# Optimization experiments

Measured on AMD Instinct MI355X. Metric: run time of the kernel, lower is better.

The kernel has to match this reference:

```python
import jax, jax.numpy as jnp
import numpy as np


def setup_inputs() -> dict:
    key = jax.random.key(0)
    z = jax.random.normal(key, (8, 4096, 1024), dtype=jnp.float32)
    return {"z": z}


def reference(z):
    d = z.shape[-1]
    # sort descending along last dim
    z_sorted = -jnp.sort(-z, axis=-1)
    z_cumsum = jnp.cumsum(z_sorted, axis=-1)
    k = jnp.arange(1, d + 1, dtype=z.dtype)  # [d]
    rhs = 1 + k * z_sorted
    is_gt = (rhs > z_cumsum).astype(z.dtype)
    # largest k satisfying the support condition
    k_z = jnp.max(is_gt * k, axis=-1, keepdims=True)  # [..., 1]
    idx = k_z.astype(jnp.int32) - 1
    z_cumsum_k = jnp.take_along_axis(z_cumsum, idx, axis=-1)
    tau = (z_cumsum_k - 1) / k_z
    p = jnp.clip(z - tau, 0.0, None)
    return p
```

## Files before the change

kernel.cpp:

```cpp
#include <hip/hip_runtime.h>


#define ROW_D 1024

typedef float f4 __attribute__((ext_vector_type(4)));

template <int CTRL, int RMASK>
__device__ __forceinline__ float dpp_mv(float x) {
    return __builtin_bit_cast(float, __builtin_amdgcn_update_dpp(
        __builtin_bit_cast(int, x), __builtin_bit_cast(int, x),
        CTRL, RMASK, 0xf, false));
}

__device__ __forceinline__ float dpp_sum_to63(float x) {
    x += dpp_mv<0x111, 0xf>(x);
    x += dpp_mv<0x112, 0xf>(x);
    x += dpp_mv<0x114, 0xf>(x);
    x += dpp_mv<0x118, 0xf>(x);
    x += dpp_mv<0x142, 0xa>(x);
    x += dpp_mv<0x143, 0xc>(x);
    return x;
}
__device__ __forceinline__ float dpp_max_to63(float x) {
    x = fmaxf(x, dpp_mv<0x111, 0xf>(x));
    x = fmaxf(x, dpp_mv<0x112, 0xf>(x));
    x = fmaxf(x, dpp_mv<0x114, 0xf>(x));
    x = fmaxf(x, dpp_mv<0x118, 0xf>(x));
    x = fmaxf(x, dpp_mv<0x142, 0xa>(x));
    x = fmaxf(x, dpp_mv<0x143, 0xc>(x));
    return x;
}
__device__ __forceinline__ float bcast63(float x) {
    return __builtin_bit_cast(float,
        __builtin_amdgcn_readlane(__builtin_bit_cast(int, x), 63));
}
__device__ __forceinline__ float fast_rcp(float x) {
    float r;
    asm("v_rcp_f32 %0, %1" : "=v"(r) : "v"(x));
    return r;
}

__device__ __forceinline__ void ce(float& a, float& b) {
    const float hi = fmaxf(a, b);
    const float lo = fminf(a, b);
    a = hi; b = lo;
}
__device__ __forceinline__ void sort4(float& a, float& b, float& c, float& d) {
    ce(a, b); ce(c, d); ce(a, c); ce(b, d); ce(b, c);
}
__device__ __forceinline__ void merge44_top4(
    float A0, float A1, float A2, float A3,
    float B0, float B1, float B2, float B3,
    float& R0, float& R1, float& R2, float& R3) {
    float e0 = A0, e1 = A2, e2 = B0, e3 = B2;
    ce(e0, e2); ce(e1, e3); ce(e1, e2);
    float o0 = A1, o1 = A3, o2 = B1, o3 = B3;
    ce(o0, o2); ce(o1, o3); ce(o1, o2);
    R0 = e0;
    float x = o0, y = e1;
    ce(x, y);
    R1 = x; R2 = y;
    R3 = fmaxf(o1, e2);
}

__global__ __launch_bounds__(256) void sparsemax_kernel(
    const float* __restrict__ z, float* __restrict__ out, int nrows) {
    const int lane = (int)(threadIdx.x & 63u);
    const int row  = (int)(blockIdx.x << 2) + (int)(threadIdx.x >> 6);
    if (row >= nrows) return;

    const f4* __restrict__ zin = reinterpret_cast<const f4*>(z + (size_t)row * ROW_D);
    f4* __restrict__ pout      = reinterpret_cast<f4*>(out + (size_t)row * ROW_D);

    f4 v[4];
#pragma unroll
    for (int j = 0; j < 4; ++j) v[j] = zin[lane + 64 * j];

    float g[4][4];
#pragma unroll
    for (int j = 0; j < 4; ++j) {
        g[j][0] = v[j].x; g[j][1] = v[j].y; g[j][2] = v[j].z; g[j][3] = v[j].w;
        sort4(g[j][0], g[j][1], g[j][2], g[j][3]);
    }
    float a0, a1, a2, a3, b0, b1, b2, b3, T0, T1, T2, T3;
    merge44_top4(g[0][0], g[0][1], g[0][2], g[0][3],
                 g[1][0], g[1][1], g[1][2], g[1][3], a0, a1, a2, a3);
    merge44_top4(g[2][0], g[2][1], g[2][2], g[2][3],
                 g[3][0], g[3][1], g[3][2], g[3][3], b0, b1, b2, b3);
    merge44_top4(a0, a1, a2, a3, b0, b1, b2, b3, T0, T1, T2, T3);

    const float m = bcast63(dpp_max_to63(T0));
    float t = m - 1.0f;

    const unsigned long long bad = __ballot(T3 > t);
    if (bad == 0ull) {
#pragma unroll 1
        for (int it = 0; it < 16; ++it) {
            const float d0 = T0 - t, d1 = T1 - t, d2 = T2 - t, d3 = T3 - t;
            const float Sl = (fmaxf(d0, 0.0f) + fmaxf(d1, 0.0f)) +
                             (fmaxf(d2, 0.0f) + fmaxf(d3, 0.0f));
            int n = __popcll(__ballot(d0 > 0.0f));
            n += __popcll(__ballot(d1 > 0.0f));
            n += __popcll(__ballot(d2 > 0.0f));
            n += __popcll(__ballot(d3 > 0.0f));
            const float S = bcast63(dpp_sum_to63(Sl));
            const float step = (S - 1.0f) * fast_rcp((float)n);
            t += step;
            if (step <= 1e-6f) break;
        }
    } else {
#pragma unroll 1
        for (int it = 0; it < 16; ++it) {
            float sj[4];
            int n = 0;
#pragma unroll
            for (int j = 0; j < 4; ++j) {
                const float d0 = v[j].x - t, d1 = v[j].y - t;
                const float d2 = v[j].z - t, d3 = v[j].w - t;
                sj[j] = (fmaxf(d0, 0.0f) + fmaxf(d1, 0.0f)) +
                        (fmaxf(d2, 0.0f) + fmaxf(d3, 0.0f));
                n += __popcll(__ballot(d0 > 0.0f));
                n += __popcll(__ballot(d1 > 0.0f));
                n += __popcll(__ballot(d2 > 0.0f));
                n += __popcll(__ballot(d3 > 0.0f));
            }
            const float S = bcast63(dpp_sum_to63((sj[0] + sj[1]) + (sj[2] + sj[3])));
            const float step = (S - 1.0f) * fast_rcp((float)n);
            t += step;
            if (step <= 1e-6f) break;
        }
    }

#pragma unroll
    for (int j = 0; j < 4; ++j) {
        f4 o;
        o.x = fmaxf(v[j].x - t, 0.0f);
        o.y = fmaxf(v[j].y - t, 0.0f);
        o.z = fmaxf(v[j].z - t, 0.0f);
        o.w = fmaxf(v[j].w - t, 0.0f);
        pout[lane + 64 * j] = o;
    }
}

extern "C" void kernel_launch(void* const* d_in, const int* in_sizes, int n_in,
                              void* d_out, int out_size, void* d_ws, size_t ws_size,
                              hipStream_t stream) {
    const float* z = (const float*)d_in[0];
    float* out = (float*)d_out;
    const int n = in_sizes[0];
    const int nrows = n / ROW_D;
    const int blocks = (nrows + 3) / 4;
    sparsemax_kernel<<<blocks, 256, 0, stream>>>(z, out, nrows);
}
```

Before: 226.6 us.

## Map each row to a 16-lane group instead of a full wavefront

New measurement: 238.7 us. 5.3% more time.

```diff
diff --git a/kernel.cpp b/kernel.cpp
--- a/kernel.cpp
+++ b/kernel.cpp
@@ -12,27 +12,24 @@
         CTRL, RMASK, 0xf, false));
 }
 
-__device__ __forceinline__ float dpp_sum_to63(float x) {
+__device__ __forceinline__ float grp_bcast15(float x) {
+    return __builtin_bit_cast(float, __builtin_amdgcn_ds_swizzle(
+        __builtin_bit_cast(int, x), 0x1F0));
+}
+
+__device__ __forceinline__ float grp_sum16(float x) {
     x += dpp_mv<0x111, 0xf>(x);
     x += dpp_mv<0x112, 0xf>(x);
     x += dpp_mv<0x114, 0xf>(x);
     x += dpp_mv<0x118, 0xf>(x);
-    x += dpp_mv<0x142, 0xa>(x);
-    x += dpp_mv<0x143, 0xc>(x);
-    return x;
+    return grp_bcast15(x);
 }
-__device__ __forceinline__ float dpp_max_to63(float x) {
+__device__ __forceinline__ float grp_max16(float x) {
     x = fmaxf(x, dpp_mv<0x111, 0xf>(x));
     x = fmaxf(x, dpp_mv<0x112, 0xf>(x));
     x = fmaxf(x, dpp_mv<0x114, 0xf>(x));
     x = fmaxf(x, dpp_mv<0x118, 0xf>(x));
-    x = fmaxf(x, dpp_mv<0x142, 0xa>(x));
-    x = fmaxf(x, dpp_mv<0x143, 0xc>(x));
-    return x;
-}
-__device__ __forceinline__ float bcast63(float x) {
-    return __builtin_bit_cast(float,
-        __builtin_amdgcn_readlane(__builtin_bit_cast(int, x), 63));
+    return grp_bcast15(x);
 }
 __device__ __forceinline__ float fast_rcp(float x) {
     float r;
@@ -66,79 +63,74 @@
 __global__ __launch_bounds__(256) void sparsemax_kernel(
     const float* __restrict__ z, float* __restrict__ out, int nrows) {
     const int lane = (int)(threadIdx.x & 63u);
-    const int row  = (int)(blockIdx.x << 2) + (int)(threadIdx.x >> 6);
+    const int g    = lane >> 4;
+    const int p    = lane & 15;
+    const int wid  = (int)(blockIdx.x << 2) + (int)(threadIdx.x >> 6);
+    const int row  = (wid << 2) + g;
     if (row >= nrows) return;
 
-    const f4* __restrict__ zin = reinterpret_cast<const f4*>(z + (size_t)row * ROW_D);
-    f4* __restrict__ pout      = reinterpret_cast<f4*>(out + (size_t)row * ROW_D);
+    const f4* __restrict__ zrow = reinterpret_cast<const f4*>(z + (size_t)row * ROW_D);
+    f4* __restrict__ prow       = reinterpret_cast<f4*>(out + (size_t)row * ROW_D);
 
-    f4 v[4];
+    f4 v[16];
 #pragma unroll
-    for (int j = 0; j < 4; ++j) v[j] = zin[lane + 64 * j];
+    for (int j = 0; j < 16; ++j) v[j] = zrow[p + 16 * j];
 
-    float g[4][4];
+    float R0 = v[0].x, R1 = v[0].y, R2 = v[0].z, R3 = v[0].w;
+    sort4(R0, R1, R2, R3);
 #pragma unroll
-    for (int j = 0; j < 4; ++j) {
-        g[j][0] = v[j].x; g[j][1] = v[j].y; g[j][2] = v[j].z; g[j][3] = v[j].w;
-        sort4(g[j][0], g[j][1], g[j][2], g[j][3]);
+    for (int j = 1; j < 16; ++j) {
+        float c0 = v[j].x, c1 = v[j].y, c2 = v[j].z, c3 = v[j].w;
+        sort4(c0, c1, c2, c3);
+        merge44_top4(R0, R1, R2, R3, c0, c1, c2, c3, R0, R1, R2, R3);
     }
-    float a0, a1, a2, a3, b0, b1, b2, b3, T0, T1, T2, T3;
-    merge44_top4(g[0][0], g[0][1], g[0][2], g[0][3],
-                 g[1][0], g[1][1], g[1][2], g[1][3], a0, a1, a2, a3);
-    merge44_top4(g[2][0], g[2][1], g[2][2], g[2][3],
-                 g[3][0], g[3][1], g[3][2], g[3][3], b0, b1, b2, b3);
-    merge44_top4(a0, a1, a2, a3, b0, b1, b2, b3, T0, T1, T2, T3);
 
-    const float m = bcast63(dpp_max_to63(T0));
+    const float m = grp_max16(R0);
     float t = m - 1.0f;
 
-    const unsigned long long bad = __ballot(T3 > t);
-    if (bad == 0ull) {
+    if (__ballot(R3 > t) == 0ull) {
 #pragma unroll 1
         for (int it = 0; it < 16; ++it) {
-            const float d0 = T0 - t, d1 = T1 - t, d2 = T2 - t, d3 = T3 - t;
+            const float d0 = R0 - t, d1 = R1 - t, d2 = R2 - t, d3 = R3 - t;
             const float Sl = (fmaxf(d0, 0.0f) + fmaxf(d1, 0.0f)) +
                              (fmaxf(d2, 0.0f) + fmaxf(d3, 0.0f));
-            int n = __popcll(__ballot(d0 > 0.0f));
-            n += __popcll(__ballot(d1 > 0.0f));
-            n += __popcll(__ballot(d2 > 0.0f));
-            n += __popcll(__ballot(d3 > 0.0f));
-            const float S = bcast63(dpp_sum_to63(Sl));
-            const float step = (S - 1.0f) * fast_rcp((float)n);
+            const float Cl = ((d0 > 0.0f ? 1.0f : 0.0f) + (d1 > 0.0f ? 1.0f : 0.0f)) +
+                             ((d2 > 0.0f ? 1.0f : 0.0f) + (d3 > 0.0f ? 1.0f : 0.0f));
+            const float S = grp_sum16(Sl);
+            const float C = grp_sum16(Cl);
+            const float step = (S - 1.0f) * fast_rcp(C);
             t += step;
-            if (step <= 1e-6f) break;
+            if (__ballot(step > 1e-6f) == 0ull) break;
         }
     } else {
 #pragma unroll 1
         for (int it = 0; it < 16; ++it) {
-            float sj[4];
-            int n = 0;
+            float Sl = 0.0f, Cl = 0.0f;
 #pragma unroll
-            for (int j = 0; j < 4; ++j) {
+            for (int j = 0; j < 16; ++j) {
                 const float d0 = v[j].x - t, d1 = v[j].y - t;
                 const float d2 = v[j].z - t, d3 = v[j].w - t;
-                sj[j] = (fmaxf(d0, 0.0f) + fmaxf(d1, 0.0f)) +
-                        (fmaxf(d2, 0.0f) + fmaxf(d3, 0.0f));
-                n += __popcll(__ballot(d0 > 0.0f));
-                n += __popcll(__ballot(d1 > 0.0f));
-                n += __popcll(__ballot(d2 > 0.0f));
-                n += __popcll(__ballot(d3 > 0.0f));
+                Sl += (fmaxf(d0, 0.0f) + fmaxf(d1, 0.0f)) +
+                      (fmaxf(d2, 0.0f) + fmaxf(d3, 0.0f));
+                Cl += ((d0 > 0.0f ? 1.0f : 0.0f) + (d1 > 0.0f ? 1.0f : 0.0f)) +
+                      ((d2 > 0.0f ? 1.0f : 0.0f) + (d3 > 0.0f ? 1.0f : 0.0f));
             }
-            const float S = bcast63(dpp_sum_to63((sj[0] + sj[1]) + (sj[2] + sj[3])));
-            const float step = (S - 1.0f) * fast_rcp((float)n);
+            const float S = grp_sum16(Sl);
+            const float C = grp_sum16(Cl);
+            const float step = (S - 1.0f) * fast_rcp(C);
             t += step;
-            if (step <= 1e-6f) break;
+            if (__ballot(step > 1e-6f) == 0ull) break;
         }
     }
 
 #pragma unroll
-    for (int j = 0; j < 4; ++j) {
+    for (int j = 0; j < 16; ++j) {
         f4 o;
         o.x = fmaxf(v[j].x - t, 0.0f);
         o.y = fmaxf(v[j].y - t, 0.0f);
         o.z = fmaxf(v[j].z - t, 0.0f);
         o.w = fmaxf(v[j].w - t, 0.0f);
-        pout[lane + 64 * j] = o;
+        prow[p + 16 * j] = o;
     }
 }
 
@@ -149,6 +141,6 @@
     float* out = (float*)d_out;
     const int n = in_sizes[0];
     const int nrows = n / ROW_D;
-    const int blocks = (nrows + 3) / 4;
+    const int blocks = (nrows + 15) / 16;
     sparsemax_kernel<<<blocks, 256, 0, stream>>>(z, out, nrows);
 }
```

## Make kernel persistent with async global-to-LDS double-buffered row prefetch

Applied to the files above, without the earlier changes.

After: 229.9 us. No clear change (+1.5%).

```diff
diff --git a/kernel.cpp b/kernel.cpp
--- a/kernel.cpp
+++ b/kernel.cpp
@@ -63,19 +63,20 @@
     R3 = fmaxf(o1, e2);
 }
 
-__global__ __launch_bounds__(256) void sparsemax_kernel(
-    const float* __restrict__ z, float* __restrict__ out, int nrows) {
-    const int lane = (int)(threadIdx.x & 63u);
-    const int row  = (int)(blockIdx.x << 2) + (int)(threadIdx.x >> 6);
-    if (row >= nrows) return;
-
-    const f4* __restrict__ zin = reinterpret_cast<const f4*>(z + (size_t)row * ROW_D);
-    f4* __restrict__ pout      = reinterpret_cast<f4*>(out + (size_t)row * ROW_D);
-
-    f4 v[4];
-#pragma unroll
-    for (int j = 0; j < 4; ++j) v[j] = zin[lane + 64 * j];
-
+__device__ __forceinline__ void prefetch_row(const float* __restrict__ z,
+                                             int row, int lane,
+                                             float* ldsbase) {
+    const char* g = (const char*)(z + (size_t)row * ROW_D) + (size_t)lane * 16;
+#pragma unroll
+    for (int j = 0; j < 4; ++j) {
+        __builtin_amdgcn_global_load_lds(
+            (const __attribute__((address_space(1))) void*)(g + j * 1024),
+            (__attribute__((address_space(3))) void*)(ldsbase + j * 256),
+            16, 0, 0);
+    }
+}
+
+__device__ __forceinline__ float solve_tau(const f4 (&v)[4]) {
     float g[4][4];
 #pragma unroll
     for (int j = 0; j < 4; ++j) {
@@ -92,8 +93,7 @@
     const float m = bcast63(dpp_max_to63(T0));
     float t = m - 1.0f;
 
-    const unsigned long long bad = __ballot(T3 > t);
-    if (bad == 0ull) {
+    if (__ballot(T3 > t) == 0ull) {
 #pragma unroll 1
         for (int it = 0; it < 16; ++it) {
             const float d0 = T0 - t, d1 = T1 - t, d2 = T2 - t, d3 = T3 - t;
@@ -130,7 +130,13 @@
             if (step <= 1e-6f) break;
         }
     }
-
+    return t;
+}
+
+__device__ __forceinline__ void store_row(const f4 (&v)[4], float t,
+                                          float* __restrict__ out,
+                                          int row, int lane) {
+    f4* __restrict__ p = reinterpret_cast<f4*>(out + (size_t)row * ROW_D);
 #pragma unroll
     for (int j = 0; j < 4; ++j) {
         f4 o;
@@ -138,7 +144,47 @@
         o.y = fmaxf(v[j].y - t, 0.0f);
         o.z = fmaxf(v[j].z - t, 0.0f);
         o.w = fmaxf(v[j].w - t, 0.0f);
-        pout[lane + 64 * j] = o;
+        p[lane + 64 * j] = o;
+    }
+}
+
+__global__ __launch_bounds__(256) void sparsemax_kernel(
+    const float* __restrict__ z, float* __restrict__ out, int nrows) {
+    const int lane = (int)(threadIdx.x & 63u);
+    const int w    = (int)(threadIdx.x >> 6);
+    int r = (int)(blockIdx.x << 2) + w;
+    const int W = (int)(gridDim.x << 2);
+    if (r >= nrows) return;
+
+    __shared__ float lds[4][2][ROW_D];
+
+    f4 v[4];
+    {
+        const f4* __restrict__ zin = reinterpret_cast<const f4*>(z + (size_t)r * ROW_D);
+#pragma unroll
+        for (int j = 0; j < 4; ++j) v[j] = zin[lane + 64 * j];
+    }
+    int rn = r + W;
+    int s = 0;
+    if (rn < nrows) prefetch_row(z, rn, lane, &lds[w][0][0]);
+    __builtin_amdgcn_sched_barrier(0);
+
+    for (;;) {
+        const float t = solve_tau(v);
+        const int rf = rn + W;
+        if (rn < nrows && rf < nrows)
+            prefetch_row(z, rf, lane, &lds[w][s ^ 1][0]);
+        __builtin_amdgcn_sched_barrier(0);
+        store_row(v, t, out, r, lane);
+        if (rn >= nrows) break;
+
+        asm volatile("s_waitcnt vmcnt(8)" ::: "memory");
+        __builtin_amdgcn_sched_barrier(0);
+        const f4* lsrc = reinterpret_cast<const f4*>(&lds[w][s][0]);
+#pragma unroll
+        for (int j = 0; j < 4; ++j) v[j] = lsrc[lane + 64 * j];
+
+        r = rn; rn = rf; s ^= 1;
     }
 }
 
@@ -149,6 +195,8 @@
     float* out = (float*)d_out;
     const int n = in_sizes[0];
     const int nrows = n / ROW_D;
-    const int blocks = (nrows + 3) / 4;
+    int blocks = 512;
+    const int max_blocks = (nrows + 3) >> 2;
+    if (blocks > max_blocks) blocks = max_blocks;
     sparsemax_kernel<<<blocks, 256, 0, stream>>>(z, out, nrows);
 }
```
